# Optimization experiments

Hardware: AMD Instinct MI355X
Metric: run time of the kernel (lower is better)

Reference implementation:

```python
import jax, jax.numpy as jnp
import numpy as np

TOPK = 2048


def setup_inputs() -> dict:
    key = jax.random.key(0)
    ks = jax.random.split(key, 16)
    M = 20000
    boxes = jax.random.uniform(ks[0], (M, 4), dtype=jnp.float32)
    scores = jax.random.uniform(ks[1], (M,), dtype=jnp.float32)
    classes = jax.random.randint(ks[2], (M,), 0, 80, dtype=jnp.int64)
    def lin(k, fan_in, fan_out):
        b = 1.0 / np.sqrt(fan_in)
        kw, kb = jax.random.split(k)
        w = jax.random.uniform(kw, (fan_in, fan_out), jnp.float32, -b, b)
        bias = jax.random.uniform(kb, (fan_out,), jnp.float32, -b, b)
        return w, bias
    sup_w1, sup_b1 = lin(ks[3], 7, 32)
    sup_w2, sup_b2 = lin(ks[4], 32, 16)
    sup_w3, sup_b3 = lin(ks[5], 16, 1)
    lam_w1, lam_b1 = lin(ks[6], 5, 16)
    lam_w2, lam_b2 = lin(ks[7], 16, 1)
    return {
        'boxes': boxes, 'scores': scores, 'classes': classes,
        'sup_w1': sup_w1, 'sup_b1': sup_b1, 'sup_w2': sup_w2, 'sup_b2': sup_b2,
        'sup_w3': sup_w3, 'sup_b3': sup_b3,
        'lam_w1': lam_w1, 'lam_b1': lam_b1, 'lam_w2': lam_w2, 'lam_b2': lam_b2,
    }


def _box_iou(b):
    # b: [N,4] in (x, y, w, h)
    x, y, w, h = b[:, 0], b[:, 1], b[:, 2], b[:, 3]
    area = w * h
    ix1 = jnp.maximum(x[:, None], x[None, :])
    iy1 = jnp.maximum(y[:, None], y[None, :])
    ix2 = jnp.minimum((x + w)[:, None], (x + w)[None, :])
    iy2 = jnp.minimum((y + h)[:, None], (y + h)[None, :])
    inter = jnp.clip(ix2 - ix1, 0) * jnp.clip(iy2 - iy1, 0)
    union = area[:, None] + area[None, :] - inter
    return inter / (union + 1e-06)


def _dacs(boxes, scores, classes,
          sup_w1, sup_b1, sup_w2, sup_b2, sup_w3, sup_b3,
          lam_w1, lam_b1, lam_w2, lam_b2):
    k = min(TOPK, scores.shape[0])
    top_scores, idx = jax.lax.top_k(scores, k)
    b = boxes[idx]            # [N,4]
    cls = classes[idx]        # [N]
    N = k
    iou = _box_iou(b)         # [N,N]
    D = iou.mean(axis=1)      # [N]
    x, y, w, h = b[:, 0], b[:, 1], b[:, 2], b[:, 3]
    feats = jnp.stack([
        iou,
        jnp.abs(x[:, None] - x[None, :]),
        jnp.abs(y[:, None] - y[None, :]),
        jnp.abs(w[:, None] - w[None, :]),
        jnp.abs(h[:, None] - h[None, :]),
        jnp.broadcast_to(top_scores[:, None], (N, N)),
        jnp.broadcast_to(top_scores[None, :], (N, N)),
    ], axis=-1)               # [N,N,7]
    hdn = jax.nn.relu(feats @ sup_w1 + sup_b1)       # [N,N,32]
    hdn = jax.nn.relu(hdn @ sup_w2 + sup_b2)         # [N,N,16]
    s_ij = jax.nn.sigmoid((hdn @ sup_w3 + sup_b3)[..., 0])  # [N,N]
    class_mask = (cls[:, None] == cls[None, :]).astype(s_ij.dtype)
    s_ij = s_ij * class_mask
    lam_in = jnp.concatenate([b, top_scores[:, None]], axis=1)  # [N,5]
    lam_h = jax.nn.relu(lam_in @ lam_w1 + lam_b1)
    lam = jax.nn.sigmoid((lam_h @ lam_w2 + lam_b2)[:, 0])       # [N]
    S = jnp.sum(s_ij * iou, axis=1)
    E = lam * S * D
    new_scores = top_scores * jnp.exp(-E)
    return b, new_scores, cls


def reference(boxes, scores, classes,
              sup_w1, sup_b1, sup_w2, sup_b2, sup_w3, sup_b3,
              lam_w1, lam_b1, lam_w2, lam_b2):
    return _dacs(boxes, scores, classes,
                 sup_w1, sup_b1, sup_w2, sup_b2, sup_w3, sup_b3,
                 lam_w1, lam_b1, lam_w2, lam_b2)
```

## Files before the change

### kernel.cpp

```cpp
#include <hip/hip_runtime.h>
#include <math.h>

#define TOPK 2048
#define NCLS 80
#define NBIN 1024
#define CMAX 2560
#define TN   512
#define CROWS 4

struct P {
    const float* scores; const float* boxes; const int* classes;
    const float* sw1; const float* sb1; const float* sw2; const float* sb2;
    const float* sw3; const float* sb3;
    const float* lw1; const float* lb1; const float* lw2; const float* lb2;
    int M; int K;
    float* out_boxes; float* out_scores; float* out_cls;
};

__device__ __forceinline__ float iou_of(float xi, float yi, float ai,
                                        float x2i, float y2i, float4 bj) {
    float ix1 = fmaxf(xi, bj.x), iy1 = fmaxf(yi, bj.y);
    float ix2 = fminf(x2i, bj.x + bj.z), iy2 = fminf(y2i, bj.y + bj.w);
    float iw = fmaxf(ix2 - ix1, 0.0f), ih = fmaxf(iy2 - iy1, 0.0f);
    float inter = iw * ih;
    float uni = ai + bj.z * bj.w - inter;
    return inter / (uni + 1e-6f);
}

__device__ __forceinline__ int digest10(float s) {
    int v = (int)(s * 1024.0f);
    return v < 0 ? 0 : (v > NBIN - 1 ? NBIN - 1 : v);
}

__device__ __forceinline__ float key_score(unsigned long long kk) {
    unsigned mono = (unsigned)(kk >> 32);
    unsigned ob = (mono & 0x80000000u) ? (mono & 0x7FFFFFFFu) : ~mono;
    return __uint_as_float(ob);
}

__global__ __launch_bounds__(TN, 4) void k_dacs(P p) {
    __shared__ int   bincur[NBIN];
    __shared__ unsigned long long skeys[CMAX];
    __shared__ int   sfx[TN];
    __shared__ int   wsum[TN / 64];
    __shared__ int   sh_cT;
    __shared__ float4 sbox[TOPK];
    __shared__ float  sscore[TOPK];
    __shared__ short  scls[TOPK];
    __shared__ short  clist[TOPK];
    __shared__ int    ccnt[NCLS], ccur[NCLS], cstart[NCLS + 1];
    __shared__ int    wtot;
    __shared__ float  swt[914];
    __shared__ float  wpart[TN / 64];
    __shared__ int    rowc[CROWS];
    __shared__ int    prefix[CROWS + 1];
    __shared__ float  Ssum[CROWS], Drow[CROWS];

    int tid = threadIdx.x, bid = blockIdx.x;
    int M = p.M, K = p.K, M4 = M >> 2;
    int r0 = bid * CROWS;
    int nrows = K - r0; if (nrows > CROWS) nrows = CROWS;
    if (nrows <= 0) return;

    for (int t = tid; t < 224; t += TN) swt[t] = p.sw1[t];
    if (tid < 32) swt[224 + tid] = p.sb1[tid];
    for (int t = tid; t < 512; t += TN) swt[256 + t] = p.sw2[t];
    if (tid < 16) swt[768 + tid] = p.sb2[tid];
    if (tid < 16) swt[784 + tid] = p.sw3[tid];
    if (tid == 0) swt[800] = p.sb3[0];
    if (tid < 80) swt[801 + tid] = p.lw1[tid];
    if (tid < 16) swt[881 + tid] = p.lb1[tid];
    if (tid < 16) swt[897 + tid] = p.lw2[tid];
    if (tid == 0) swt[913] = p.lb2[0];

    for (int b = tid; b < NBIN; b += TN) bincur[b] = 0;
    if (tid < NCLS) ccnt[tid] = 0;
    if (tid < CROWS) Ssum[tid] = 0.0f;
    __syncthreads();

    const float4* s4p = (const float4*)p.scores;
    for (int i4 = tid; i4 < M4; i4 += TN) {
        float4 v = s4p[i4];
        atomicAdd(&bincur[digest10(v.x)], 1);
        atomicAdd(&bincur[digest10(v.y)], 1);
        atomicAdd(&bincur[digest10(v.z)], 1);
        atomicAdd(&bincur[digest10(v.w)], 1);
    }
    for (int i = M4 * 4 + tid; i < M; i += TN)
        atomicAdd(&bincur[digest10(p.scores[i])], 1);
    __syncthreads();

    {
        const int BPT = NBIN / TN;
        int c0 = tid * BPT, sum = 0;
        #pragma unroll
        for (int u = 0; u < BPT; u++) sum += bincur[c0 + u];
        int lane = tid & 63;
        int x = sum;
        #pragma unroll
        for (int off = 1; off < 64; off <<= 1) {
            int v = __shfl_down(x, off, 64);
            if (lane + off < 64) x += v;
        }
        if (lane == 0) wsum[tid >> 6] = x;
        __syncthreads();
        if (tid < TN / 64) {
            int t = wsum[tid];
            #pragma unroll
            for (int off = 1; off < TN / 64; off <<= 1) {
                int v = __shfl_down(t, off, 64);
                if (tid + off < TN / 64) t += v;
            }
            wsum[tid] = t;
        }
        __syncthreads();
        int wid = tid >> 6;
        int higher = (wid < TN / 64 - 1) ? wsum[wid + 1] : 0;
        sfx[tid] = x + higher;
    }
    __syncthreads();

    {
        const int BPT = NBIN / TN;
        int running = (tid < TN - 1) ? sfx[tid + 1] : 0;
        int c0 = tid * BPT;
        for (int u = BPT - 1; u >= 0; u--) {
            int b = c0 + u, cnt = bincur[b];
            if (running < K && running + cnt >= K) sh_cT = b;
            bincur[b] = (running << 13);
            running += cnt;
        }
    }
    __syncthreads();
    int cT = sh_cT;

    for (int i4 = tid; i4 < M4; i4 += TN) {
        float4 v = s4p[i4];
        #pragma unroll
        for (int u = 0; u < 4; u++) {
            float s = (u == 0) ? v.x : (u == 1) ? v.y : (u == 2) ? v.z : v.w;
            int d = digest10(s);
            if (d >= cT) {
                int i = i4 * 4 + u;
                int old = atomicAdd(&bincur[d], 1);
                int slot = (old >> 13) + (old & 8191);
                if (slot < CMAX) {
                    unsigned b = __float_as_uint(s);
                    b = (b & 0x80000000u) ? ~b : (b | 0x80000000u);
                    skeys[slot] = ((unsigned long long)b << 32) |
                                  (unsigned long long)(0xFFFFFFFFu - (unsigned)i);
                }
            }
        }
    }
    for (int i = M4 * 4 + tid; i < M; i += TN) {
        float s = p.scores[i];
        int d = digest10(s);
        if (d >= cT) {
            int old = atomicAdd(&bincur[d], 1);
            int slot = (old >> 13) + (old & 8191);
            if (slot < CMAX) {
                unsigned b = __float_as_uint(s);
                b = (b & 0x80000000u) ? ~b : (b | 0x80000000u);
                skeys[slot] = ((unsigned long long)b << 32) |
                              (unsigned long long)(0xFFFFFFFFu - (unsigned)i);
            }
        }
    }
    __syncthreads();

    int pkT = bincur[cT];
    int C = (pkT >> 13) + (pkT & 8191); if (C > CMAX) C = CMAX;
    {
        const float4* boxes4 = (const float4*)p.boxes;
        for (int s = tid; s < C; s += TN) {
            unsigned long long ks = skeys[s];
            unsigned idx = 0xFFFFFFFFu - (unsigned)(ks & 0xFFFFFFFFull);
            float sc = key_score(ks);
            int d = digest10(sc);
            int pk = bincur[d];
            int st = pk >> 13;
            int en = st + (pk & 8191); if (en > CMAX) en = CMAX;
            int r = st;
            for (int t = st; t < en; t++) r += (skeys[t] > ks) ? 1 : 0;
            if (r < K) {
                sbox[r] = boxes4[idx];
                sscore[r] = sc;
                scls[r] = (short)p.classes[idx];
            }
        }
    }
    __syncthreads();

    for (int r = tid; r < K; r += TN) atomicAdd(&ccnt[scls[r]], 1);
    __syncthreads();
    {
        int x = 0, v = 0;
        if (tid < 128) {
            v = (tid < NCLS) ? ccnt[tid] : 0;
            x = v;
            #pragma unroll
            for (int off = 1; off < 64; off <<= 1) {
                int t = __shfl_up(x, off, 64);
                if ((tid & 63) >= off) x += t;
            }
            if (tid == 63) wtot = x;
        }
        __syncthreads();
        if (tid < NCLS) {
            int excl = x - v + ((tid >= 64) ? wtot : 0);
            ccur[tid] = excl;
            cstart[tid] = excl;
        }
        if (tid == 0) cstart[NCLS] = K;
        __syncthreads();
        for (int r = tid; r < K; r += TN) {
            int pos = atomicAdd(&ccur[scls[r]], 1);
            clist[pos] = (short)r;
        }
    }
    __syncthreads();

    {
        int wv = tid >> 6, lane = tid & 63;
        int row = wv >> 1, half = wv & 1;
        float dsum = 0.0f;
        if (row < nrows) {
            float4 bi = sbox[r0 + row];
            float ai = bi.z * bi.w, x2i = bi.x + bi.z, y2i = bi.y + bi.w;
            for (int j = lane + (half << 6); j < K; j += 128)
                dsum += iou_of(bi.x, bi.y, ai, x2i, y2i, sbox[j]);
            #pragma unroll
            for (int off = 32; off >= 1; off >>= 1)
                dsum += __shfl_xor(dsum, off, 64);
        }
        if (lane == 0) wpart[wv] = dsum;
    }

    if (tid < CROWS) {
        int st = 0, cnt = 0;
        if (tid < nrows) {
            int c = scls[r0 + tid];
            st = cstart[c];
            cnt = cstart[c + 1] - st;
        }
        rowc[tid] = st;
        prefix[tid] = cnt;
    }
    __syncthreads();
    if (tid < nrows) Drow[tid] = (wpart[2 * tid] + wpart[2 * tid + 1]) / (float)K;
    if (tid == 0) {
        int acc = 0;
        #pragma unroll
        for (int rr = 0; rr < CROWS; rr++) { int t = prefix[rr]; prefix[rr] = acc; acc += t; }
        prefix[CROWS] = acc;
    }
    __syncthreads();

    int Pb = prefix[CROWS];
    const float* W1 = swt;       const float* B1 = swt + 224;
    const float* W2 = swt + 256; const float* B2 = swt + 768;
    const float* W3 = swt + 784; float B3 = swt[800];

    for (int pp = tid; pp < Pb; pp += TN) {
        int lo = 0, hi = CROWS;
        while (hi - lo > 1) {
            int mid = (lo + hi) >> 1;
            if (prefix[mid] <= pp) lo = mid; else hi = mid;
        }
        int row = lo;
        int j = (int)clist[rowc[row] + (pp - prefix[row])];
        float4 bi = sbox[r0 + row];
        float4 bj = sbox[j];
        float ai = bi.z * bi.w, x2i = bi.x + bi.z, y2i = bi.y + bi.w;
        float iou = iou_of(bi.x, bi.y, ai, x2i, y2i, bj);
        float f1 = fabsf(bi.x - bj.x), f2 = fabsf(bi.y - bj.y);
        float f3 = fabsf(bi.z - bj.z), f4 = fabsf(bi.w - bj.w);
        float f5 = sscore[r0 + row], f6 = sscore[j];
        float acc2[16];
        #pragma unroll
        for (int q = 0; q < 16; q++) acc2[q] = B2[q];
        #pragma unroll 2
        for (int o = 0; o < 32; o++) {
            float a = B1[o];
            a += iou * W1[0 * 32 + o];
            a += f1 * W1[1 * 32 + o];
            a += f2 * W1[2 * 32 + o];
            a += f3 * W1[3 * 32 + o];
            a += f4 * W1[4 * 32 + o];
            a += f5 * W1[5 * 32 + o];
            a += f6 * W1[6 * 32 + o];
            float h = fmaxf(a, 0.0f);
            #pragma unroll
            for (int q = 0; q < 16; q++) acc2[q] += h * W2[o * 16 + q];
        }
        float acc3 = B3;
        #pragma unroll
        for (int q = 0; q < 16; q++) acc3 += fmaxf(acc2[q], 0.0f) * W3[q];
        atomicAdd(&Ssum[row], iou / (1.0f + expf(-acc3)));
    }
    __syncthreads();

    if (tid < nrows) {
        int r = r0 + tid;
        float4 bi = sbox[r];
        float si = sscore[r];
        const float* LW1 = swt + 801; const float* LB1 = swt + 881;
        const float* LW2 = swt + 897; float LB2 = swt[913];
        float in5[5] = { bi.x, bi.y, bi.z, bi.w, si };
        float acc = LB2;
        #pragma unroll
        for (int o = 0; o < 16; o++) {
            float a2 = LB1[o];
            #pragma unroll
            for (int f = 0; f < 5; f++) a2 += in5[f] * LW1[f * 16 + o];
            acc += fmaxf(a2, 0.0f) * LW2[o];
        }
        float lam = 1.0f / (1.0f + expf(-acc));
        ((float4*)p.out_boxes)[r] = bi;
        p.out_cls[r] = (float)scls[r];
        p.out_scores[r] = si * expf(-lam * Ssum[tid] * Drow[tid]);
    }
}

extern "C" void kernel_launch(void* const* d_in, const int* in_sizes, int n_in,
                              void* d_out, int out_size, void* d_ws, size_t ws_size,
                              hipStream_t stream) {
    int M = in_sizes[1];
    int K = (M < TOPK) ? M : TOPK;

    P dp;
    dp.scores  = (const float*)d_in[1];
    dp.boxes   = (const float*)d_in[0];
    dp.classes = (const int*)d_in[2];
    dp.sw1 = (const float*)d_in[3];  dp.sb1 = (const float*)d_in[4];
    dp.sw2 = (const float*)d_in[5];  dp.sb2 = (const float*)d_in[6];
    dp.sw3 = (const float*)d_in[7];  dp.sb3 = (const float*)d_in[8];
    dp.lw1 = (const float*)d_in[9];  dp.lb1 = (const float*)d_in[10];
    dp.lw2 = (const float*)d_in[11]; dp.lb2 = (const float*)d_in[12];
    dp.M = M; dp.K = K;
    dp.out_boxes  = (float*)d_out;
    dp.out_scores = (float*)d_out + (size_t)K * 4;
    dp.out_cls    = (float*)d_out + (size_t)K * 5;

    int nb = (K + CROWS - 1) / CROWS;
    k_dacs<<<nb, TN, 0, stream>>>(dp);
}
```

Before: 110.3 us.

## Hoist score histogram into single-block pre-kernel and widen bins

Splits the histogram and threshold-bin search out of the per-row fused kernel into a separate single-block kernel that writes bin offsets and the cutoff bin to workspace. Each of the 512 fused blocks then loads the precomputed offsets instead of re-histogramming all 20000 scores. It also doubles the bin count to shrink the candidate set and in-bin rank loops, and restructures the D row-mean so all waves process four rows at once. It adds a kernel launch and a serial single-block dependency, and the fused blocks still rescan all scores for scatter.

```diff
diff --git a/kernel.cpp b/kernel.cpp
--- a/kernel.cpp
+++ b/kernel.cpp
@@ -3,13 +3,18 @@
 
 #define TOPK 2048
 #define NCLS 80
-#define NBIN 1024
-#define CMAX 2560
+#define NBIN 2048
+#define CMAX 2176
+#define TNA  1024
 #define TN   512
 #define CROWS 4
 
-struct P {
+
+struct HistP { const float* scores; int M; int K; int* ghist; int* gmeta; };
+
+struct FusP {
     const float* scores; const float* boxes; const int* classes;
+    const int* ghist; const int* gmeta;
     const float* sw1; const float* sb1; const float* sw2; const float* sb2;
     const float* sw3; const float* sb3;
     const float* lw1; const float* lb1; const float* lw2; const float* lb2;
@@ -27,9 +32,16 @@
     return inter / (uni + 1e-6f);
 }
 
-__device__ __forceinline__ int digest10(float s) {
-    int v = (int)(s * 1024.0f);
+__device__ __forceinline__ int digest11(float s) {
+    int v = (int)(s * 2048.0f);
     return v < 0 ? 0 : (v > NBIN - 1 ? NBIN - 1 : v);
+}
+
+__device__ __forceinline__ unsigned long long make_key(float s, unsigned i) {
+    unsigned b = __float_as_uint(s);
+    b = (b & 0x80000000u) ? ~b : (b | 0x80000000u);
+    return ((unsigned long long)b << 32) |
+           (unsigned long long)(0xFFFFFFFFu - i);
 }
 
 __device__ __forceinline__ float key_score(unsigned long long kk) {
@@ -38,20 +50,86 @@
     return __uint_as_float(ob);
 }
 
-__global__ __launch_bounds__(TN, 4) void k_dacs(P p) {
-    __shared__ int   bincur[NBIN];
+__global__ __launch_bounds__(TNA, 1) void k_hist(HistP p) {
+    __shared__ int lbin[NBIN];
+    __shared__ int sfx[TNA];
+    __shared__ int wsum[TNA / 64];
+    __shared__ int sh_cT;
+
+    int tid = threadIdx.x;
+    int M = p.M, K = p.K, M4 = M >> 2;
+
+    for (int b = tid; b < NBIN; b += TNA) lbin[b] = 0;
+    __syncthreads();
+
+    const float4* s4p = (const float4*)p.scores;
+    for (int i4 = tid; i4 < M4; i4 += TNA) {
+        float4 v = s4p[i4];
+        atomicAdd(&lbin[digest11(v.x)], 1);
+        atomicAdd(&lbin[digest11(v.y)], 1);
+        atomicAdd(&lbin[digest11(v.z)], 1);
+        atomicAdd(&lbin[digest11(v.w)], 1);
+    }
+    for (int i = M4 * 4 + tid; i < M; i += TNA)
+        atomicAdd(&lbin[digest11(p.scores[i])], 1);
+    __syncthreads();
+
+    {
+        const int BPT = NBIN / TNA;
+        int c0 = tid * BPT, sum = 0;
+        #pragma unroll
+        for (int u = 0; u < BPT; u++) sum += lbin[c0 + u];
+        int lane = tid & 63;
+        int x = sum;
+        #pragma unroll
+        for (int off = 1; off < 64; off <<= 1) {
+            int v = __shfl_down(x, off, 64);
+            if (lane + off < 64) x += v;
+        }
+        if (lane == 0) wsum[tid >> 6] = x;
+        __syncthreads();
+        if (tid < TNA / 64) {
+            int t = wsum[tid];
+            #pragma unroll
+            for (int off = 1; off < TNA / 64; off <<= 1) {
+                int v = __shfl_down(t, off, 64);
+                if (tid + off < TNA / 64) t += v;
+            }
+            wsum[tid] = t;
+        }
+        __syncthreads();
+        int wid = tid >> 6;
+        int higher = (wid < TNA / 64 - 1) ? wsum[wid + 1] : 0;
+        sfx[tid] = x + higher;
+    }
+    __syncthreads();
+
+    {
+        const int BPT = NBIN / TNA;
+        int running = (tid < TNA - 1) ? sfx[tid + 1] : 0;
+        int c0 = tid * BPT;
+        for (int u = BPT - 1; u >= 0; u--) {
+            int b = c0 + u, cnt = lbin[b];
+            if (running < K && running + cnt >= K) sh_cT = b;
+            p.ghist[b] = (running << 16);
+            running += cnt;
+        }
+    }
+    __syncthreads();
+    if (tid == 0) p.gmeta[0] = sh_cT;
+}
+
+__global__ __launch_bounds__(TN, 4) void k_fused(FusP p) {
+    __shared__ int    bincur[NBIN];
     __shared__ unsigned long long skeys[CMAX];
-    __shared__ int   sfx[TN];
-    __shared__ int   wsum[TN / 64];
-    __shared__ int   sh_cT;
     __shared__ float4 sbox[TOPK];
     __shared__ float  sscore[TOPK];
     __shared__ short  scls[TOPK];
     __shared__ short  clist[TOPK];
-    __shared__ int    ccnt[NCLS], ccur[NCLS], cstart[NCLS + 1];
+    __shared__ int    cstart[NCLS + 1], ccnt[NCLS], ccur[NCLS];
     __shared__ int    wtot;
     __shared__ float  swt[914];
-    __shared__ float  wpart[TN / 64];
+    __shared__ float  wpart[(TN / 64) * CROWS];
     __shared__ int    rowc[CROWS];
     __shared__ int    prefix[CROWS + 1];
     __shared__ float  Ssum[CROWS], Drow[CROWS];
@@ -72,115 +150,51 @@
     if (tid < 16) swt[881 + tid] = p.lb1[tid];
     if (tid < 16) swt[897 + tid] = p.lw2[tid];
     if (tid == 0) swt[913] = p.lb2[0];
-
-    for (int b = tid; b < NBIN; b += TN) bincur[b] = 0;
+    for (int b = tid; b < NBIN; b += TN) bincur[b] = p.ghist[b];
     if (tid < NCLS) ccnt[tid] = 0;
     if (tid < CROWS) Ssum[tid] = 0.0f;
     __syncthreads();
+
+    int cT = p.gmeta[0];
 
     const float4* s4p = (const float4*)p.scores;
     for (int i4 = tid; i4 < M4; i4 += TN) {
         float4 v = s4p[i4];
-        atomicAdd(&bincur[digest10(v.x)], 1);
-        atomicAdd(&bincur[digest10(v.y)], 1);
-        atomicAdd(&bincur[digest10(v.z)], 1);
-        atomicAdd(&bincur[digest10(v.w)], 1);
-    }
-    for (int i = M4 * 4 + tid; i < M; i += TN)
-        atomicAdd(&bincur[digest10(p.scores[i])], 1);
-    __syncthreads();
-
-    {
-        const int BPT = NBIN / TN;
-        int c0 = tid * BPT, sum = 0;
-        #pragma unroll
-        for (int u = 0; u < BPT; u++) sum += bincur[c0 + u];
-        int lane = tid & 63;
-        int x = sum;
-        #pragma unroll
-        for (int off = 1; off < 64; off <<= 1) {
-            int v = __shfl_down(x, off, 64);
-            if (lane + off < 64) x += v;
-        }
-        if (lane == 0) wsum[tid >> 6] = x;
-        __syncthreads();
-        if (tid < TN / 64) {
-            int t = wsum[tid];
-            #pragma unroll
-            for (int off = 1; off < TN / 64; off <<= 1) {
-                int v = __shfl_down(t, off, 64);
-                if (tid + off < TN / 64) t += v;
-            }
-            wsum[tid] = t;
-        }
-        __syncthreads();
-        int wid = tid >> 6;
-        int higher = (wid < TN / 64 - 1) ? wsum[wid + 1] : 0;
-        sfx[tid] = x + higher;
-    }
-    __syncthreads();
-
-    {
-        const int BPT = NBIN / TN;
-        int running = (tid < TN - 1) ? sfx[tid + 1] : 0;
-        int c0 = tid * BPT;
-        for (int u = BPT - 1; u >= 0; u--) {
-            int b = c0 + u, cnt = bincur[b];
-            if (running < K && running + cnt >= K) sh_cT = b;
-            bincur[b] = (running << 13);
-            running += cnt;
-        }
-    }
-    __syncthreads();
-    int cT = sh_cT;
-
-    for (int i4 = tid; i4 < M4; i4 += TN) {
-        float4 v = s4p[i4];
         #pragma unroll
         for (int u = 0; u < 4; u++) {
             float s = (u == 0) ? v.x : (u == 1) ? v.y : (u == 2) ? v.z : v.w;
-            int d = digest10(s);
+            int d = digest11(s);
             if (d >= cT) {
-                int i = i4 * 4 + u;
                 int old = atomicAdd(&bincur[d], 1);
-                int slot = (old >> 13) + (old & 8191);
-                if (slot < CMAX) {
-                    unsigned b = __float_as_uint(s);
-                    b = (b & 0x80000000u) ? ~b : (b | 0x80000000u);
-                    skeys[slot] = ((unsigned long long)b << 32) |
-                                  (unsigned long long)(0xFFFFFFFFu - (unsigned)i);
-                }
+                int slot = (old >> 16) + (old & 0xFFFF);
+                if (slot < CMAX)
+                    skeys[slot] = make_key(s, (unsigned)(i4 * 4 + u));
             }
         }
     }
     for (int i = M4 * 4 + tid; i < M; i += TN) {
         float s = p.scores[i];
-        int d = digest10(s);
+        int d = digest11(s);
         if (d >= cT) {
             int old = atomicAdd(&bincur[d], 1);
-            int slot = (old >> 13) + (old & 8191);
-            if (slot < CMAX) {
-                unsigned b = __float_as_uint(s);
-                b = (b & 0x80000000u) ? ~b : (b | 0x80000000u);
-                skeys[slot] = ((unsigned long long)b << 32) |
-                              (unsigned long long)(0xFFFFFFFFu - (unsigned)i);
-            }
+            int slot = (old >> 16) + (old & 0xFFFF);
+            if (slot < CMAX) skeys[slot] = make_key(s, (unsigned)i);
         }
     }
     __syncthreads();
 
     int pkT = bincur[cT];
-    int C = (pkT >> 13) + (pkT & 8191); if (C > CMAX) C = CMAX;
+    int C = (pkT >> 16) + (pkT & 0xFFFF); if (C > CMAX) C = CMAX;
     {
         const float4* boxes4 = (const float4*)p.boxes;
         for (int s = tid; s < C; s += TN) {
             unsigned long long ks = skeys[s];
             unsigned idx = 0xFFFFFFFFu - (unsigned)(ks & 0xFFFFFFFFull);
             float sc = key_score(ks);
-            int d = digest10(sc);
+            int d = digest11(sc);
             int pk = bincur[d];
-            int st = pk >> 13;
-            int en = st + (pk & 8191); if (en > CMAX) en = CMAX;
+            int st = pk >> 16;
+            int en = st + (pk & 0xFFFF); if (en > CMAX) en = CMAX;
             int r = st;
             for (int t = st; t < en; t++) r += (skeys[t] > ks) ? 1 : 0;
             if (r < K) {
@@ -222,19 +236,36 @@
     __syncthreads();
 
     {
-        int wv = tid >> 6, lane = tid & 63;
-        int row = wv >> 1, half = wv & 1;
-        float dsum = 0.0f;
-        if (row < nrows) {
-            float4 bi = sbox[r0 + row];
-            float ai = bi.z * bi.w, x2i = bi.x + bi.z, y2i = bi.y + bi.w;
-            for (int j = lane + (half << 6); j < K; j += 128)
-                dsum += iou_of(bi.x, bi.y, ai, x2i, y2i, sbox[j]);
-            #pragma unroll
-            for (int off = 32; off >= 1; off >>= 1)
-                dsum += __shfl_xor(dsum, off, 64);
-        }
-        if (lane == 0) wpart[wv] = dsum;
+        float4 b0 = sbox[r0];
+        float4 b1 = (nrows > 1) ? sbox[r0 + 1] : b0;
+        float4 b2 = (nrows > 2) ? sbox[r0 + 2] : b0;
+        float4 b3 = (nrows > 3) ? sbox[r0 + 3] : b0;
+        float a0 = b0.z * b0.w, x20 = b0.x + b0.z, y20 = b0.y + b0.w;
+        float a1 = b1.z * b1.w, x21 = b1.x + b1.z, y21 = b1.y + b1.w;
+        float a2 = b2.z * b2.w, x22 = b2.x + b2.z, y22 = b2.y + b2.w;
+        float a3 = b3.z * b3.w, x23 = b3.x + b3.z, y23 = b3.y + b3.w;
+        float d0 = 0.0f, d1 = 0.0f, d2 = 0.0f, d3 = 0.0f;
+        for (int j = tid; j < K; j += TN) {
+            float4 bj = sbox[j];
+            d0 += iou_of(b0.x, b0.y, a0, x20, y20, bj);
+            d1 += iou_of(b1.x, b1.y, a1, x21, y21, bj);
+            d2 += iou_of(b2.x, b2.y, a2, x22, y22, bj);
+            d3 += iou_of(b3.x, b3.y, a3, x23, y23, bj);
+        }
+        #pragma unroll
+        for (int off = 32; off >= 1; off >>= 1) {
+            d0 += __shfl_xor(d0, off, 64);
+            d1 += __shfl_xor(d1, off, 64);
+            d2 += __shfl_xor(d2, off, 64);
+            d3 += __shfl_xor(d3, off, 64);
+        }
+        int lane = tid & 63, wv = tid >> 6;
+        if (lane == 0) {
+            wpart[wv * CROWS + 0] = d0;
+            wpart[wv * CROWS + 1] = d1;
+            wpart[wv * CROWS + 2] = d2;
+            wpart[wv * CROWS + 3] = d3;
+        }
     }
 
     if (tid < CROWS) {
@@ -248,7 +279,12 @@
         prefix[tid] = cnt;
     }
     __syncthreads();
-    if (tid < nrows) Drow[tid] = (wpart[2 * tid] + wpart[2 * tid + 1]) / (float)K;
+    if (tid < nrows) {
+        float s = 0.0f;
+        #pragma unroll
+        for (int wv = 0; wv < TN / 64; wv++) s += wpart[wv * CROWS + tid];
+        Drow[tid] = s / (float)K;
+    }
     if (tid == 0) {
         int acc = 0;
         #pragma unroll
@@ -263,12 +299,7 @@
     const float* W3 = swt + 784; float B3 = swt[800];
 
     for (int pp = tid; pp < Pb; pp += TN) {
-        int lo = 0, hi = CROWS;
-        while (hi - lo > 1) {
-            int mid = (lo + hi) >> 1;
-            if (prefix[mid] <= pp) lo = mid; else hi = mid;
-        }
-        int row = lo;
+        int row = (pp >= prefix[1]) + (pp >= prefix[2]) + (pp >= prefix[3]);
         int j = (int)clist[rowc[row] + (pp - prefix[row])];
         float4 bi = sbox[r0 + row];
         float4 bj = sbox[j];
@@ -329,20 +360,29 @@
     int M = in_sizes[1];
     int K = (M < TOPK) ? M : TOPK;
 
-    P dp;
-    dp.scores  = (const float*)d_in[1];
-    dp.boxes   = (const float*)d_in[0];
-    dp.classes = (const int*)d_in[2];
-    dp.sw1 = (const float*)d_in[3];  dp.sb1 = (const float*)d_in[4];
-    dp.sw2 = (const float*)d_in[5];  dp.sb2 = (const float*)d_in[6];
-    dp.sw3 = (const float*)d_in[7];  dp.sb3 = (const float*)d_in[8];
-    dp.lw1 = (const float*)d_in[9];  dp.lb1 = (const float*)d_in[10];
-    dp.lw2 = (const float*)d_in[11]; dp.lb2 = (const float*)d_in[12];
-    dp.M = M; dp.K = K;
-    dp.out_boxes  = (float*)d_out;
-    dp.out_scores = (float*)d_out + (size_t)K * 4;
-    dp.out_cls    = (float*)d_out + (size_t)K * 5;
-
-    int nb = (K + CROWS - 1) / CROWS;
-    k_dacs<<<nb, TN, 0, stream>>>(dp);
-}
+    char* ws = (char*)d_ws;
+    int* ghist = (int*)ws;                     ws += (size_t)NBIN * 4;
+    int* gmeta = (int*)ws;                     ws += 16;
+
+    HistP hp;
+    hp.scores = (const float*)d_in[1];
+    hp.M = M; hp.K = K; hp.ghist = ghist; hp.gmeta = gmeta;
+
+    FusP fp;
+    fp.scores  = (const float*)d_in[1];
+    fp.boxes   = (const float*)d_in[0];
+    fp.classes = (const int*)d_in[2];
+    fp.ghist = ghist; fp.gmeta = gmeta;
+    fp.sw1 = (const float*)d_in[3];  fp.sb1 = (const float*)d_in[4];
+    fp.sw2 = (const float*)d_in[5];  fp.sb2 = (const float*)d_in[6];
+    fp.sw3 = (const float*)d_in[7];  fp.sb3 = (const float*)d_in[8];
+    fp.lw1 = (const float*)d_in[9];  fp.lb1 = (const float*)d_in[10];
+    fp.lw2 = (const float*)d_in[11]; fp.lb2 = (const float*)d_in[12];
+    fp.M = M; fp.K = K;
+    fp.out_boxes  = (float*)d_out;
+    fp.out_scores = (float*)d_out + (size_t)K * 4;
+    fp.out_cls    = (float*)d_out + (size_t)K * 5;
+
+    k_hist<<<1, TNA, 0, stream>>>(hp);
+    k_fused<<<(K + CROWS - 1) / CROWS, TN, 0, stream>>>(fp);
+}
```

After: 111.8 us. About the same (+1.4%).
